# Kernel optimization log

Hardware: AMD Instinct MI355X
Metric: run time of the kernel (lower is better)

Reference implementation:

```python
import jax, jax.numpy as jnp
import numpy as np

KS = 3   # window kernel size
NH = 4   # num heads

def unfold3d(x, ks):
    # x: (B,C,D,H,W) -> (B,C,D*H*W, ks**3); matches torch unfold(2).unfold(3).unfold(4) ordering
    B, C, D, H, W = x.shape
    p = ks // 2
    xp = jnp.pad(x, ((0,0),(0,0),(p,p),(p,p),(p,p)))
    wins = [xp[:, :, i:i+D, j:j+H, k:k+W]
            for i in range(ks) for j in range(ks) for k in range(ks)]
    u = jnp.stack(wins, axis=-1)  # (B,C,D,H,W,ks^3)
    return u.reshape(B, C, D*H*W, ks**3)

def make_mask(D, H, W, ks):
    ones = jnp.ones((1, 1, D, H, W), jnp.float32)
    return unfold3d(ones, ks)[0, 0] == 0  # (N, ks^3), True = out-of-bounds (masked)

def l2norm(x, eps=1e-12):
    n = jnp.sqrt(jnp.sum(x * x, axis=-1, keepdims=True))
    return x / jnp.maximum(n, eps)

def layernorm(x, g, b, eps=1e-5):
    m = x.mean(-1, keepdims=True)
    v = x.var(-1, keepdims=True)
    return (x - m) / jnp.sqrt(v + eps) * g + b

def conv3d(x, w, b, pad):
    y = jax.lax.conv_general_dilated(x, w, (1,1,1), [(pad,pad)]*3,
        dimension_numbers=('NCDHW', 'OIDHW', 'NCDHW'))
    return y + b.reshape(1, -1, 1, 1, 1)

def bnorm(x, g, b, eps=1e-5):
    # BatchNorm3d, training-mode batch statistics (biased variance)
    m = x.mean(axis=(0,2,3,4), keepdims=True)
    v = ((x - m) ** 2).mean(axis=(0,2,3,4), keepdims=True)
    return (x - m) / jnp.sqrt(v + eps) * g.reshape(1,-1,1,1,1) + b.reshape(1,-1,1,1,1)

def lrelu(x):
    return jnp.where(x > 0, x, 0.01 * x)

def resblock(x, w1, b1, g1, be1, w2, b2, g2, be2):
    # monai UnetResBlock, in==out, stride 1 -> identity residual
    y = lrelu(bnorm(conv3d(x, w1, b1, 1), g1, be1))
    y = bnorm(conv3d(y, w2, b2, 1), g2, be2)
    return lrelu(y + x)

def epa(x, D, H, W, mask, qkvv_w, temp, temp2, rpb, qemb, op1_w, op1_b, op2_w, op2_b):
    B, N, C = x.shape
    hd = C // NH
    qkvv = (x @ qkvv_w.T).reshape(B, N, 4, NH, hd).transpose(2, 0, 3, 1, 4)  # (4,B,NH,N,hd)
    q, k, v_ca, v_sa = qkvv[0], qkvv[1], qkvv[2], qkvv[3]
    # ---- spatial (local window) attention ----
    qns = (l2norm(q) + qemb) * jax.nn.softplus(temp2)  # (B,NH,N,hd)
    k_flat = k.transpose(0, 1, 3, 2).reshape(B, C, N)
    v_flat = v_sa.transpose(0, 1, 3, 2).reshape(B, C, N)
    k_loc = unfold3d(k_flat.reshape(B, C, D, H, W), KS).reshape(B, NH, hd, N, KS**3).transpose(0, 1, 3, 2, 4)
    v_loc = unfold3d(v_flat.reshape(B, C, D, H, W), KS).reshape(B, NH, hd, N, KS**3).transpose(0, 1, 3, 2, 4)
    attn_sa = jnp.einsum('bhnd,bhndk->bhnk', qns, k_loc) + rpb[None, :, None, :]
    attn_sa = jnp.where(mask[None, None], -jnp.inf, attn_sa)
    attn_sa = jax.nn.softmax(attn_sa, axis=-1)
    # NOTE: original torch code reshapes (B,NH,N,hd) directly to (B,N,C); replicate exactly
    x_sa = jnp.einsum('bhnk,bhndk->bhnd', attn_sa, v_loc).reshape(B, N, C)
    # ---- channel (cosine) cross-attention ----
    qt = l2norm(q.transpose(0, 1, 3, 2))  # (B,NH,hd,N), normalized over N
    kt = l2norm(k.transpose(0, 1, 3, 2))
    attn_ca = jax.nn.softmax(jnp.einsum('bhdn,bhen->bhde', qt, kt) * temp, axis=-1)
    x_ca = jnp.einsum('bhde,bhen->bhdn', attn_ca, v_ca.transpose(0, 1, 3, 2)).transpose(0, 3, 1, 2).reshape(B, N, C)
    return jnp.concatenate([x_sa @ op1_w.T + op1_b, x_ca @ op2_w.T + op2_b], axis=-1)


def setup_inputs() -> dict:
    key = jax.random.key(0)
    B, C, H, W, D = 1, 64, 32, 32, 32
    hd = C // NH
    ks = iter(jax.random.split(key, 40))
    def nrm(shape, s=0.02):
        return jax.random.normal(next(ks), shape, jnp.float32) * s
    inp = {
        'x': jax.random.normal(next(ks), (B, C, H, W, D), jnp.float32),
        'ln_g': jnp.ones((C,), jnp.float32), 'ln_b': jnp.zeros((C,), jnp.float32),
        'gamma': 1e-6 * jnp.ones((C,), jnp.float32),
        'qkvv_w': nrm((4 * C, C)),
        'temp': jnp.ones((NH, 1, 1), jnp.float32), 'temp2': jnp.ones((NH, 1, 1), jnp.float32),
        'rpb': nrm((NH, KS**3), 4e-4),
        'qemb': nrm((NH, 1, hd)),
        'op1_w': nrm((C // 2, C)), 'op1_b': jnp.zeros((C // 2,), jnp.float32),
        'op2_w': nrm((C // 2, C)), 'op2_b': jnp.zeros((C // 2,), jnp.float32),
    }
    for name in ('c51', 'c52'):
        inp[name + '_w1'] = nrm((C, C, 3, 3, 3)); inp[name + '_b1'] = jnp.zeros((C,), jnp.float32)
        inp[name + '_g1'] = jnp.ones((C,), jnp.float32); inp[name + '_be1'] = jnp.zeros((C,), jnp.float32)
        inp[name + '_w2'] = nrm((C, C, 3, 3, 3)); inp[name + '_b2'] = jnp.zeros((C,), jnp.float32)
        inp[name + '_g2'] = jnp.ones((C,), jnp.float32); inp[name + '_be2'] = jnp.zeros((C,), jnp.float32)
    inp['c8_w'] = nrm((C, C, 1, 1, 1)); inp['c8_b'] = jnp.zeros((C,), jnp.float32)
    return inp


def reference(x, ln_g, ln_b, gamma, qkvv_w, temp, temp2, rpb, qemb,
              op1_w, op1_b, op2_w, op2_b,
              c51_w1, c51_b1, c51_g1, c51_be1, c51_w2, c51_b2, c51_g2, c51_be2,
              c52_w1, c52_b1, c52_g1, c52_be1, c52_w2, c52_b2, c52_g2, c52_be2,
              c8_w, c8_b):
    B, C, H, W, D = x.shape
    N = H * W * D
    xs = x.reshape(B, C, N).transpose(0, 2, 1)  # (B,N,C)
    mask = make_mask(D, H, W, KS)
    attn = xs + gamma * epa(layernorm(xs, ln_g, ln_b), D, H, W, mask,
                            qkvv_w, temp, temp2, rpb, qemb, op1_w, op1_b, op2_w, op2_b)
    skip = attn.reshape(B, H, W, D, C).transpose(0, 4, 1, 2, 3)  # (B,C,H,W,D)
    y = resblock(skip, c51_w1, c51_b1, c51_g1, c51_be1, c51_w2, c51_b2, c51_g2, c51_be2)
    y = resblock(y, c52_w1, c52_b1, c52_g1, c52_be1, c52_w2, c52_b2, c52_g2, c52_be2)
    return skip + conv3d(y, c8_w, c8_b, 0)
```

## Files before the change

kernel.cpp:

```cpp
#include <hip/hip_runtime.h>
#include <hip/hip_bf16.h>

typedef __hip_bfloat16 bf16;
typedef __attribute__((ext_vector_type(8))) short s8v;
typedef __attribute__((ext_vector_type(4))) float f4v;

#define NTOT 32768
#define HSZ ((size_t)NTOT*16)

__device__ __forceinline__ float bflo(unsigned int u){ union{unsigned int i;float f;}v; v.i=u<<16; return v.f; }
__device__ __forceinline__ float bfhi(unsigned int u){ union{unsigned int i;float f;}v; v.i=u&0xffff0000u; return v.f; }
__device__ __forceinline__ unsigned short f2bu(float f){ bf16 h = __float2bfloat16(f); unsigned short s; __builtin_memcpy(&s,&h,2); return s; }
__device__ __forceinline__ unsigned int pk2(float a, float b){ return (unsigned int)f2bu(a) | ((unsigned int)f2bu(b)<<16); }

__device__ __forceinline__ void load16(const bf16* p, float* o){
  const uint4* q = (const uint4*)p;
  uint4 u0 = q[0], u1 = q[1];
  o[0]=bflo(u0.x); o[1]=bfhi(u0.x); o[2]=bflo(u0.y); o[3]=bfhi(u0.y);
  o[4]=bflo(u0.z); o[5]=bfhi(u0.z); o[6]=bflo(u0.w); o[7]=bfhi(u0.w);
  o[8]=bflo(u1.x); o[9]=bfhi(u1.x); o[10]=bflo(u1.y); o[11]=bfhi(u1.y);
  o[12]=bflo(u1.z); o[13]=bfhi(u1.z); o[14]=bflo(u1.w); o[15]=bfhi(u1.w);
}

__global__ __launch_bounds__(256) void k_qkvv(const float* __restrict__ x,
    const float* __restrict__ lng, const float* __restrict__ lnb,
    const float* __restrict__ w,
    bf16* __restrict__ Qh, bf16* __restrict__ Kh, bf16* __restrict__ Vsh, bf16* __restrict__ Vch)
{
  __shared__ unsigned char sm[64000];
  float* xt = (float*)sm;
  float* mean_s = (float*)(sm + 16896);
  float* rstd_s = (float*)(sm + 16896 + 256);
  float* g_s    = (float*)(sm + 16896 + 512);
  float* b_s    = (float*)(sm + 16896 + 768);
  unsigned char* A2 = sm + 17920;
  unsigned char* Wb = sm + 27136;
  unsigned char* Cout = sm;

  int t = threadIdx.x;
  int n0 = blockIdx.x * 64;
  #pragma unroll
  for (int i=0;i<4;i++){
    int idx = t + i*256; int c = idx>>4, g = idx&15;
    *(float4*)&xt[c*66 + g*4] = *(const float4*)(x + (size_t)c*NTOT + n0 + g*4);
  }
  #pragma unroll
  for (int i=0;i<8;i++){
    int idx = t + i*256; int j = idx>>3, g = idx&7;
    float4 wa = *(const float4*)(w + (size_t)j*64 + g*8);
    float4 wb = *(const float4*)(w + (size_t)j*64 + g*8 + 4);
    uint4 u; u.x=pk2(wa.x,wa.y); u.y=pk2(wa.z,wa.w); u.z=pk2(wb.x,wb.y); u.w=pk2(wb.z,wb.w);
    *(uint4*)(Wb + j*144 + g*16) = u;
  }
  if (t<64){ g_s[t]=lng[t]; b_s[t]=lnb[t]; }
  __syncthreads();
  if (t<64){
    float s=0.f, ss=0.f;
    for (int c=0;c<64;c++){ float v=xt[c*66+t]; s+=v; ss+=v*v; }
    float m = s*(1.f/64.f);
    float var = ss*(1.f/64.f) - m*m;
    mean_s[t]=m; rstd_s[t]=rsqrtf(var+1e-5f);
  }
  __syncthreads();
  {
    int p = t>>2, c0 = (t&3)*16;
    float m = mean_s[p], rs = rstd_s[p];
    unsigned short tmp[16];
    #pragma unroll
    for (int i=0;i<16;i++){
      int c = c0+i;
      tmp[i] = f2bu((xt[c*66+p]-m)*rs*g_s[c] + b_s[c]);
    }
    *(uint4*)(A2 + p*144 + c0*2)      = *(uint4*)&tmp[0];
    *(uint4*)(A2 + p*144 + c0*2 + 16) = *(uint4*)&tmp[8];
  }
  __syncthreads();
  int wv = t>>6, lane = t&63, r = lane&15, q = lane>>4;
  f4v acc[4][4];
  #pragma unroll
  for (int mt=0;mt<4;mt++)
    #pragma unroll
    for (int nt=0;nt<4;nt++){ acc[mt][nt][0]=0.f; acc[mt][nt][1]=0.f; acc[mt][nt][2]=0.f; acc[mt][nt][3]=0.f; }
  #pragma unroll
  for (int ks=0; ks<2; ++ks){
    s8v af[4], bfr[4];
    #pragma unroll
    for (int mt=0;mt<4;mt++) af[mt] = *(const s8v*)(A2 + (mt*16+r)*144 + ks*64 + q*16);
    #pragma unroll
    for (int nt=0;nt<4;nt++) bfr[nt] = *(const s8v*)(Wb + ((wv*4+nt)*16+r)*144 + ks*64 + q*16);
    #pragma unroll
    for (int mt=0;mt<4;mt++)
      #pragma unroll
      for (int nt=0;nt<4;nt++)
        acc[mt][nt] = __builtin_amdgcn_mfma_f32_16x16x32_bf16(af[mt], bfr[nt], acc[mt][nt], 0, 0, 0);
  }
  __syncthreads();
  #pragma unroll
  for (int mt=0;mt<4;mt++)
    #pragma unroll
    for (int nt=0;nt<4;nt++){
      int j = (wv*4+nt)*16 + r;
      #pragma unroll
      for (int reg=0;reg<4;reg++){
        int p = mt*16 + q*4 + reg;
        *(unsigned short*)(Cout + p*528 + j*2) = f2bu(acc[mt][nt][reg]);
      }
    }
  __syncthreads();
  bf16* bases[4] = {Qh, Kh, Vch, Vsh};
  #pragma unroll
  for (int k=0;k<4;k++){
    int chunk = t + k*256;
    int combo = chunk >> 6, pos = chunk & 63;
    int tensor = combo >> 2, h = combo & 3;
    uint4 v = *(const uint4*)(Cout + pos*528 + (tensor*64 + h*16)*2);
    *(uint4*)((unsigned char*)bases[tensor] + ((size_t)h*HSZ + (size_t)(n0+pos)*16)*2) = v;
  }
}

__global__ __launch_bounds__(256) void k_chanpart(const bf16* __restrict__ Qh, const bf16* __restrict__ Kh,
    float* __restrict__ G, float* __restrict__ NQ, float* __restrict__ NK)
{
  int h = blockIdx.y;
  int t = threadIdx.x; int d = t>>4, e = t&15;
  __shared__ float qs[128][16];
  __shared__ float ks[128][16];
  float acc=0.f, accq=0.f, acck=0.f;
  for (int stage=0; stage<4; ++stage){
    int n0 = blockIdx.x*512 + stage*128;
    __syncthreads();
    {
      int row = t & 127, which = t >> 7;
      const bf16* p = (which ? Kh : Qh) + ((size_t)h*NTOT + n0 + row)*16;
      float tmp[16]; load16(p, tmp);
      float* dst = which ? &ks[row][0] : &qs[row][0];
      #pragma unroll
      for (int i=0;i<16;i++) dst[i]=tmp[i];
    }
    __syncthreads();
    for (int i=0;i<128;i++){
      float qv = qs[i][d], kv = ks[i][e];
      acc += qv*kv;
      if (e==0) accq += qv*qv;
      if (e==1){ float kd = ks[i][d]; acck += kd*kd; }
    }
  }
  atomicAdd(&G[(h*16+d)*16+e], acc);
  if (e==0) atomicAdd(&NQ[h*16+d], accq);
  if (e==1) atomicAdd(&NK[h*16+d], acck);
}

__global__ __launch_bounds__(256) void k_spatial(const bf16* __restrict__ Qh, const bf16* __restrict__ Kh,
    const bf16* __restrict__ Vsh, const bf16* __restrict__ Vch,
    const float* __restrict__ G, const float* __restrict__ NQ, const float* __restrict__ NK,
    const float* __restrict__ temp, const float* __restrict__ temp2,
    const float* __restrict__ rpb, const float* __restrict__ qemb,
    const float* __restrict__ x,
    const float* __restrict__ op1w, const float* __restrict__ op1b,
    const float* __restrict__ op2w, const float* __restrict__ op2b,
    const float* __restrict__ gamma, float* __restrict__ skipf)
{
  __shared__ float aca_s[1024];
  __shared__ float rpb_s[108];
  __shared__ float qemb_s[64];
  __shared__ float xs_s[64][68];
  __shared__ float xc_s[64][68];
  int t = threadIdx.x;
  int n0 = blockIdx.x * 64;
  if (t < 64){
    int hh = t>>4;
    float tp = temp[hh];
    float nq = fmaxf(sqrtf(NQ[t]), 1e-12f);
    float sv[16]; float mx=-3.0e38f;
    #pragma unroll
    for (int e=0;e<16;e++){
      float nk = fmaxf(sqrtf(NK[hh*16+e]), 1e-12f);
      sv[e] = G[t*16+e] / (nq*nk) * tp;
      mx = fmaxf(mx, sv[e]);
    }
    float sum=0.f;
    #pragma unroll
    for (int e=0;e<16;e++){ sv[e]=expf(sv[e]-mx); sum+=sv[e]; }
    float inv = 1.f/sum;
    #pragma unroll
    for (int e=0;e<16;e++) aca_s[t*16+e] = sv[e]*inv;
  }
  if (t<108) rpb_s[t]=rpb[t];
  if (t<64) qemb_s[t]=qemb[t];
  __syncthreads();
  int lane = t & 63, h = t >> 6;
  int n = n0 + lane;
  int a = n>>10, b=(n>>5)&31, c=n&31;
  const bf16* Kb = Kh + (size_t)h*HSZ;
  const bf16* Vb = Vsh + (size_t)h*HSZ;
  float q[16]; load16(Qh + (size_t)h*HSZ + (size_t)n*16, q);
  float s2=0.f;
  #pragma unroll
  for (int d=0;d<16;d++) s2 += q[d]*q[d];
  float inv = 1.f/fmaxf(sqrtf(s2), 1e-12f);
  float st2 = log1pf(expf(temp2[h]));
  #pragma unroll
  for (int d=0;d<16;d++) q[d] = (q[d]*inv + qemb_s[h*16+d])*st2;
  float sc[27]; float mx = -3.0e38f;
  #pragma unroll
  for (int kk=0;kk<27;kk++){
    int da=kk/9-1, db=(kk/3)%3-1, dc=kk%3-1;
    int aa=a+da, bb=b+db, cc=c+dc;
    float s = -3.0e38f;
    if ((unsigned)aa<32u && (unsigned)bb<32u && (unsigned)cc<32u){
      int nn = n + da*1024 + db*32 + dc;
      float kv[16]; load16(Kb + (size_t)nn*16, kv);
      s = rpb_s[h*27+kk];
      #pragma unroll
      for (int d=0;d<16;d++) s += q[d]*kv[d];
    }
    sc[kk]=s; mx = fmaxf(mx, s);
  }
  float sum=0.f;
  #pragma unroll
  for (int kk=0;kk<27;kk++){ float e = expf(sc[kk]-mx); sc[kk]=e; sum+=e; }
  float invs = 1.f/sum;
  float o[16];
  #pragma unroll
  for (int d=0;d<16;d++) o[d]=0.f;
  #pragma unroll
  for (int kk=0;kk<27;kk++){
    int da=kk/9-1, db=(kk/3)%3-1, dc=kk%3-1;
    int aa=a+da, bb=b+db, cc=c+dc;
    if ((unsigned)aa<32u && (unsigned)bb<32u && (unsigned)cc<32u){
      int nn = n + da*1024 + db*32 + dc;
      float vv[16]; load16(Vb + (size_t)nn*16, vv);
      float p = sc[kk];
      #pragma unroll
      for (int d=0;d<16;d++) o[d] += p*vv[d];
    }
  }
  {
    int jrow = h*16 + (lane>>2), cbase = (lane&3)*16;
    #pragma unroll
    for (int d=0;d<16;d++) xs_s[jrow][cbase + d] = o[d]*invs;
  }
  {
    float vca[16]; load16(Vch + (size_t)h*HSZ + (size_t)n*16, vca);
    #pragma unroll
    for (int d=0;d<16;d++){
      float s=0.f;
      #pragma unroll
      for (int e=0;e<16;e++) s += aca_s[(h*16+d)*16+e]*vca[e];
      xc_s[lane][h*16+d] = s;
    }
  }
  __syncthreads();
  int co = t & 63, pg = t >> 6;
  const float* wrow = (co < 32) ? (op1w + (size_t)co*64) : (op2w + (size_t)(co-32)*64);
  float wreg[64];
  #pragma unroll
  for (int i=0;i<16;i++) *(float4*)&wreg[i*4] = *(const float4*)(wrow + i*4);
  float bv = (co<32) ? op1b[co] : op2b[co-32];
  float gv = gamma[co];
  const float* xt_ = (co<32) ? &xs_s[0][0] : &xc_s[0][0];
  #pragma unroll
  for (int i=0;i<16;i++){
    int p = pg*16 + i;
    const float* xr = xt_ + p*68;
    float s = bv;
    #pragma unroll
    for (int k4=0;k4<16;k4++){
      float4 xv = *(const float4*)(xr + k4*4);
      s += wreg[k4*4]*xv.x + wreg[k4*4+1]*xv.y + wreg[k4*4+2]*xv.z + wreg[k4*4+3]*xv.w;
    }
    int m;
    if (co < 32){ int hh2 = p>>4, jj = p&15; m = hh2*8192 + (n0>>2) + jj; }
    else m = n0 + p;
    skipf[(size_t)m*64 + co] = x[(size_t)co*NTOT + m] + gv*s;
  }
}

__global__ void k_wprep(const float* __restrict__ wA, const float* __restrict__ wB_,
    const float* __restrict__ wC, const float* __restrict__ wD,
    const float* __restrict__ w8, bf16* __restrict__ WB, float* __restrict__ w8t,
    float* __restrict__ statz)
{
  int idx = blockIdx.x*256 + threadIdx.x;
  if (idx < 1152) statz[idx] = 0.f;
  if (idx < 458752){
    int j = idx & 7;
    int rr = (idx>>3) & 15;
    int q = (idx>>7) & 3;
    int nt = (idx>>9) & 3;
    int rest = idx >> 11;
    int tp = rest % 14;
    int rest2 = rest / 14;
    int cc = rest2 & 3;
    int conv = rest2 >> 2;
    int co = nt*16 + rr;
    int tap = 2*tp + (q>>1);
    int ci = cc*16 + (q&1)*8 + j;
    const float* src = conv==0?wA:conv==1?wB_:conv==2?wC:wD;
    float v = (tap < 27) ? src[((size_t)co*64 + ci)*27 + tap] : 0.f;
    WB[idx] = __float2bfloat16(v);
  }
  if (idx < 4096){ int ci = idx>>6, co = idx&63; w8t[ci*64+co] = w8[(size_t)co*64+ci]; }
}

template<int MODE>
__global__ __launch_bounds__(256, 2) void k_conv3x(const void* __restrict__ src,
    const float* __restrict__ stats, const float* __restrict__ g, const float* __restrict__ be,
    const float* __restrict__ resid,
    const bf16* __restrict__ WB, const float* __restrict__ bias,
    bf16* __restrict__ Yout, float* __restrict__ BNpart)
{
  __shared__ float smf[17408];
  unsigned char* smb = (unsigned char*)smf;
  int t = threadIdx.x;
  int w = t >> 6, lane = t & 63;
  int r = lane & 15, q = lane >> 4;
  int qe = q & 1, qh = q >> 1;
  int a = blockIdx.x >> 4, b0 = (blockIdx.x & 15) * 2;
  int hh = t & 7;

  float m8[8], rs8[8], be8[8];
  if (MODE != 0){
    #pragma unroll
    for (int i=0;i<8;i++){
      int ci = hh*8 + i;
      float S = stats[ci*2], SS = stats[ci*2+1];
      float m = S*(1.f/NTOT);
      m8[i] = m;
      rs8[i] = rsqrtf(SS*(1.f/NTOT) - m*m + 1e-5f) * g[ci];
      be8[i] = be[ci];
    }
  }

  if (MODE == 0){
    #pragma unroll
    for (int c0=0;c0<2;++c0){
      int kb = c0*7, kn = (c0==0)?7:6;
      float4 f0[7], f1[7]; int fl[7];
      #pragma unroll
      for (int k=0;k<7;k++){
        fl[k]=0;
        if (k<kn){
          int idx = t + (kb+k)*256;
          if (idx < 3264){
            int pos = idx>>3;
            int par=pos/136, rem=pos-par*136, pbr=rem/34, pc=rem-pbr*34;
            int pa=a+par, pb=b0+pbr;
            fl[k]=1;
            if (pa>=1&&pa<=32&&pb>=1&&pb<=32&&pc>=1&&pc<=32){
              int nsrc=(pa-1)*1024+(pb-1)*32+(pc-1);
              const float* p = (const float*)src + (size_t)nsrc*64 + hh*8;
              f0[k]=*(const float4*)p; f1[k]=*(const float4*)(p+4);
              fl[k]=2;
            }
          }
        }
      }
      #pragma unroll
      for (int k=0;k<7;k++){
        if (k<kn && fl[k]){
          int pos = (t + (kb+k)*256)>>3;
          uint4 o={0,0,0,0};
          if (fl[k]==2){
            o.x=pk2(f0[k].x,f0[k].y); o.y=pk2(f0[k].z,f0[k].w);
            o.z=pk2(f1[k].x,f1[k].y); o.w=pk2(f1[k].z,f1[k].w);
          }
          *(uint4*)(smb + pos*144 + hh*16) = o;
        }
      }
    }
  } else {
    const int CS = (MODE==2)?5:13;
    const int NC = (MODE==2)?3:1;
    #pragma unroll
    for (int c0=0;c0<NC;++c0){
      int kb = c0*CS;
      int kn = (MODE==2) ? ((c0==2)?3:5) : 13;
      uint4 u[CS]; float4 r0[CS], r1[CS]; int fl[CS];
      #pragma unroll
      for (int k=0;k<CS;k++){
        fl[k]=0;
        if (k<kn){
          int idx = t + (kb+k)*256;
          if (idx < 3264){
            int pos = idx>>3;
            int par=pos/136, rem=pos-par*136, pbr=rem/34, pc=rem-pbr*34;
            int pa=a+par, pb=b0+pbr;
            fl[k]=1;
            if (pa>=1&&pa<=32&&pb>=1&&pb<=32&&pc>=1&&pc<=32){
              int nsrc=(pa-1)*1024+(pb-1)*32+(pc-1);
              u[k] = *(const uint4*)((const unsigned char*)src + ((size_t)nsrc*64 + hh*8)*2);
              if (MODE==2){
                const float* rp = resid + (size_t)nsrc*64 + hh*8;
                r0[k]=*(const float4*)rp; r1[k]=*(const float4*)(rp+4);
              }
              fl[k]=2;
            }
          }
        }
      }
      #pragma unroll
      for (int k=0;k<CS;k++){
        if (k<kn && fl[k]){
          int pos = (t + (kb+k)*256)>>3;
          uint4 o={0,0,0,0};
          if (fl[k]==2){
            float v[8];
            v[0]=bflo(u[k].x); v[1]=bfhi(u[k].x); v[2]=bflo(u[k].y); v[3]=bfhi(u[k].y);
            v[4]=bflo(u[k].z); v[5]=bfhi(u[k].z); v[6]=bflo(u[k].w); v[7]=bfhi(u[k].w);
            float rv[8];
            if (MODE==2){
              rv[0]=r0[k].x; rv[1]=r0[k].y; rv[2]=r0[k].z; rv[3]=r0[k].w;
              rv[4]=r1[k].x; rv[5]=r1[k].y; rv[6]=r1[k].z; rv[7]=r1[k].w;
            }
            #pragma unroll
            for (int i=0;i<8;i++){
              float y = (v[i]-m8[i])*rs8[i] + be8[i];
              if (MODE==2) y += rv[i];
              v[i] = y>0.f ? y : 0.01f*y;
            }
            o.x=pk2(v[0],v[1]); o.y=pk2(v[2],v[3]); o.z=pk2(v[4],v[5]); o.w=pk2(v[6],v[7]);
          }
          *(uint4*)(smb + pos*144 + hh*16) = o;
        }
      }
    }
  }

  int toff[14];
  #pragma unroll
  for (int tp=0;tp<14;++tp){
    int tap = 2*tp + qh;
    int da = tap/9, rem = tap - da*9, db = rem/3, dc = rem - db*3;
    toff[tp] = (tap<27) ? (((da*4+db)*34 + dc)*144) : 0;
  }
  int F[4];
  #pragma unroll
  for (int mt=0;mt<4;mt++) F[mt] = (((mt>>1)*34 + (mt&1)*16 + r)*144) + w*32 + qe*16;
  const unsigned char* wbp = (const unsigned char*)WB + (size_t)w*57344 + lane*16;

  f4v acc[4][4];
  #pragma unroll
  for (int mt=0;mt<4;mt++)
    #pragma unroll
    for (int nt=0;nt<4;nt++){ acc[mt][nt][0]=0.f; acc[mt][nt][1]=0.f; acc[mt][nt][2]=0.f; acc[mt][nt][3]=0.f; }

  __syncthreads();

  s8v aC[4], bC[4], bN[4];
  #pragma unroll
  for (int mt=0;mt<4;mt++) aC[mt] = *(const s8v*)(smb + F[mt] + toff[0]);
  #pragma unroll
  for (int nt=0;nt<4;nt++){ bC[nt] = *(const s8v*)(wbp + nt*1024); bN[nt] = *(const s8v*)(wbp + 4096 + nt*1024); }

  #pragma unroll
  for (int tp=0; tp<14; ++tp){
    s8v aN[4], bN2[4];
    if (tp < 12){
      #pragma unroll
      for (int nt=0;nt<4;nt++) bN2[nt] = *(const s8v*)(wbp + (tp+2)*4096 + nt*1024);
    }
    if (tp < 13){
      #pragma unroll
      for (int mt=0;mt<4;mt++) aN[mt] = *(const s8v*)(smb + F[mt] + toff[tp+1]);
    }
    #pragma unroll
    for (int mt=0;mt<4;mt++)
      #pragma unroll
      for (int nt=0;nt<4;nt++)
        acc[mt][nt] = __builtin_amdgcn_mfma_f32_16x16x32_bf16(aC[mt], bC[nt], acc[mt][nt], 0, 0, 0);
    #pragma unroll
    for (int nt=0;nt<4;nt++) bC[nt] = bN[nt];
    if (tp < 12){
      #pragma unroll
      for (int nt=0;nt<4;nt++) bN[nt] = bN2[nt];
    }
    if (tp < 13){
      #pragma unroll
      for (int mt=0;mt<4;mt++) aC[mt] = aN[mt];
    }
  }

  __syncthreads();
  #pragma unroll
  for (int mt=0;mt<4;mt++)
    #pragma unroll
    for (int nt=0;nt<4;nt++)
      *(float4*)&smf[w*4352 + (nt*16+r)*68 + mt*16 + q*4] = *(float4*)&acc[mt][nt];
  __syncthreads();

  float vals[16];
  {
    int co = t >> 2, pg = t & 3;
    float bv = bias[co];
    #pragma unroll
    for (int i4=0;i4<4;i4++){
      int p = pg*16 + i4*4;
      float4 s0 = *(const float4*)&smf[0*4352 + co*68 + p];
      float4 s1 = *(const float4*)&smf[1*4352 + co*68 + p];
      float4 s2 = *(const float4*)&smf[2*4352 + co*68 + p];
      float4 s3 = *(const float4*)&smf[3*4352 + co*68 + p];
      vals[i4*4+0] = s0.x+s1.x+s2.x+s3.x+bv;
      vals[i4*4+1] = s0.y+s1.y+s2.y+s3.y+bv;
      vals[i4*4+2] = s0.z+s1.z+s2.z+s3.z+bv;
      vals[i4*4+3] = s0.w+s1.w+s2.w+s3.w+bv;
    }
    float s=0.f, ss=0.f;
    #pragma unroll
    for (int i=0;i<16;i++){ s+=vals[i]; ss+=vals[i]*vals[i]; }
    s += __shfl_xor(s,1); ss += __shfl_xor(ss,1);
    s += __shfl_xor(s,2); ss += __shfl_xor(ss,2);
    if (pg==0){
      BNpart[(size_t)blockIdx.x*128 + co*2]     = s;
      BNpart[(size_t)blockIdx.x*128 + co*2 + 1] = ss;
    }
  }
  __syncthreads();
  {
    int co = t >> 2, pg = t & 3;
    #pragma unroll
    for (int i=0;i<16;i++) smf[(pg*16+i)*68 + co] = vals[i];
  }
  __syncthreads();
  {
    int pos = t >> 2, grp = t & 3;
    float v16[16];
    #pragma unroll
    for (int i4=0;i4<4;i4++) *(float4*)&v16[i4*4] = *(const float4*)&smf[pos*68 + grp*16 + i4*4];
    uint4 u0, u1;
    u0.x=pk2(v16[0],v16[1]); u0.y=pk2(v16[2],v16[3]); u0.z=pk2(v16[4],v16[5]); u0.w=pk2(v16[6],v16[7]);
    u1.x=pk2(v16[8],v16[9]); u1.y=pk2(v16[10],v16[11]); u1.z=pk2(v16[12],v16[13]); u1.w=pk2(v16[14],v16[15]);
    int nb = a*1024 + (b0 + (pos>>5))*32 + (pos&31);
    uint4* dst = (uint4*)((unsigned char*)Yout + ((size_t)nb*64 + grp*16)*2);
    dst[0] = u0; dst[1] = u1;
  }
}

__global__ __launch_bounds__(1024) void k_bnred(const float* __restrict__ BNpart, float* __restrict__ BNout)
{
  __shared__ float red[8][128];
  int t = threadIdx.x;
  int col = t & 127, grp = t >> 7;
  float acc = 0.f;
  #pragma unroll 8
  for (int r = grp*64; r < grp*64 + 64; ++r) acc += BNpart[r*128 + col];
  red[grp][col] = acc;
  __syncthreads();
  if (grp == 0){
    float s = 0.f;
    #pragma unroll
    for (int g=0; g<8; g++) s += red[g][col];
    BNout[col] = s;
  }
}

__global__ __launch_bounds__(256) void k_conv1f(const bf16* __restrict__ Y4,
    const float* __restrict__ BN4, const float* __restrict__ g4, const float* __restrict__ be4,
    const bf16* __restrict__ Y2, const float* __restrict__ BN2,
    const float* __restrict__ g2, const float* __restrict__ be2,
    const float* __restrict__ skipf, const float* __restrict__ w8t, const float* __restrict__ b8,
    float* __restrict__ out)
{
  __shared__ float R2[64][68];
  __shared__ float skT[64][68];
  __shared__ float wt[4096];
  __shared__ float bs[64];
  int t = threadIdx.x;
  int n0 = blockIdx.x * 64;
  #pragma unroll
  for (int k=0;k<4;k++){
    int idx = t + k*256;
    *(float4*)&wt[idx*4] = *(const float4*)(w8t + idx*4);
  }
  if (t < 64) bs[t] = b8[t];
  {
    int pos = t >> 2, grp = t & 3;
    int n = n0 + pos;
    float y2[16], y4[16], sk[16];
    load16(Y2 + (size_t)n*64 + grp*16, y2);
    load16(Y4 + (size_t)n*64 + grp*16, y4);
    #pragma unroll
    for (int i4=0;i4<4;i4++) *(float4*)&sk[i4*4] = *(const float4*)(skipf + (size_t)n*64 + grp*16 + i4*4);
    #pragma unroll
    for (int i=0;i<16;i++){
      int ci = grp*16+i;
      float S2=BN2[ci*2], SS2=BN2[ci*2+1];
      float m2=S2*(1.f/NTOT);
      float r2v=rsqrtf(SS2*(1.f/NTOT)-m2*m2+1e-5f);
      float R = (y2[i]-m2)*r2v*g2[ci]+be2[ci] + sk[i];
      R = R>0.f ? R : 0.01f*R;
      float S4=BN4[ci*2], SS4=BN4[ci*2+1];
      float m4=S4*(1.f/NTOT);
      float r4v=rsqrtf(SS4*(1.f/NTOT)-m4*m4+1e-5f);
      float vy = (y4[i]-m4)*r4v*g4[ci]+be4[ci] + R;
      vy = vy>0.f ? vy : 0.01f*vy;
      R2[ci][pos] = vy;
      skT[ci][pos] = sk[i];
    }
  }
  __syncthreads();
  int lane = t & 63, cg = t >> 6;
  float acc[16];
  #pragma unroll
  for (int j=0;j<16;j++) acc[j]=0.f;
  for (int ci=0; ci<64; ci++){
    float rv = R2[ci][lane];
    const float* wr = &wt[ci*64 + cg*16];
    float4 wa = *(const float4*)(wr);
    float4 wb = *(const float4*)(wr+4);
    float4 wc = *(const float4*)(wr+8);
    float4 wd = *(const float4*)(wr+12);
    acc[0]+=rv*wa.x; acc[1]+=rv*wa.y; acc[2]+=rv*wa.z; acc[3]+=rv*wa.w;
    acc[4]+=rv*wb.x; acc[5]+=rv*wb.y; acc[6]+=rv*wb.z; acc[7]+=rv*wb.w;
    acc[8]+=rv*wc.x; acc[9]+=rv*wc.y; acc[10]+=rv*wc.z; acc[11]+=rv*wc.w;
    acc[12]+=rv*wd.x; acc[13]+=rv*wd.y; acc[14]+=rv*wd.z; acc[15]+=rv*wd.w;
  }
  #pragma unroll
  for (int j=0;j<16;j++){
    int co = cg*16+j;
    out[(size_t)co*NTOT + n0 + lane] = acc[j] + bs[co] + skT[co][lane];
  }
}

extern "C" void kernel_launch(void* const* d_in, const int* in_sizes, int n_in,
                              void* d_out, int out_size, void* d_ws, size_t ws_size,
                              hipStream_t stream) {
  (void)in_sizes; (void)n_in; (void)out_size; (void)ws_size;
  const float* x      = (const float*)d_in[0];
  const float* ln_g   = (const float*)d_in[1];
  const float* ln_b   = (const float*)d_in[2];
  const float* gamma  = (const float*)d_in[3];
  const float* qkvv_w = (const float*)d_in[4];
  const float* temp   = (const float*)d_in[5];
  const float* temp2  = (const float*)d_in[6];
  const float* rpb    = (const float*)d_in[7];
  const float* qemb   = (const float*)d_in[8];
  const float* op1w   = (const float*)d_in[9];
  const float* op1b   = (const float*)d_in[10];
  const float* op2w   = (const float*)d_in[11];
  const float* op2b   = (const float*)d_in[12];
  const float* c51_w1 = (const float*)d_in[13];
  const float* c51_b1 = (const float*)d_in[14];
  const float* c51_g1 = (const float*)d_in[15];
  const float* c51_be1= (const float*)d_in[16];
  const float* c51_w2 = (const float*)d_in[17];
  const float* c51_b2 = (const float*)d_in[18];
  const float* c51_g2 = (const float*)d_in[19];
  const float* c51_be2= (const float*)d_in[20];
  const float* c52_w1 = (const float*)d_in[21];
  const float* c52_b1 = (const float*)d_in[22];
  const float* c52_g1 = (const float*)d_in[23];
  const float* c52_be1= (const float*)d_in[24];
  const float* c52_w2 = (const float*)d_in[25];
  const float* c52_b2 = (const float*)d_in[26];
  const float* c52_g2 = (const float*)d_in[27];
  const float* c52_be2= (const float*)d_in[28];
  const float* c8_w   = (const float*)d_in[29];
  const float* c8_b   = (const float*)d_in[30];

  unsigned char* ws = (unsigned char*)d_ws;
  const size_t MB = 1u<<20;
  bf16*  Qh   = (bf16*)(ws + 0);
  bf16*  Kh   = (bf16*)(ws + 4*MB);
  bf16*  Vsh  = (bf16*)(ws + 8*MB);
  bf16*  Vch  = (bf16*)(ws + 12*MB);
  float* skipf= (float*)(ws + 24*MB);
  float* stat = (float*)(ws + 32*MB);
  float* G    = stat + 0;
  float* NQ   = stat + 1024;
  float* NK   = stat + 1088;
  float* BN1  = stat + 1152;
  float* BN2  = stat + 1312;
  float* BN3  = stat + 1472;
  float* BN4  = stat + 1632;
  bf16*  WB   = (bf16*)(ws + 33*MB);
  float* w8t  = (float*)(ws + 33*MB + 1048576);
  float* BNpart = (float*)(ws + 35*MB);
  bf16*  Y1   = (bf16*)(ws + 36*MB);
  bf16*  Y2   = (bf16*)(ws + 40*MB);
  bf16*  Y3   = (bf16*)(ws + 44*MB);
  bf16*  Y4   = (bf16*)(ws + 48*MB);

  k_wprep<<<1792,256,0,stream>>>(c51_w1, c51_w2, c52_w1, c52_w2, c8_w, WB, w8t, stat);
  k_qkvv<<<512,256,0,stream>>>(x, ln_g, ln_b, qkvv_w, Qh, Kh, Vsh, Vch);
  k_chanpart<<<dim3(64,4),256,0,stream>>>(Qh, Kh, G, NQ, NK);
  k_spatial<<<512,256,0,stream>>>(Qh, Kh, Vsh, Vch, G, NQ, NK, temp, temp2, rpb, qemb,
                                  x, op1w, op1b, op2w, op2b, gamma, skipf);
  k_conv3x<0><<<512,256,0,stream>>>(skipf, nullptr, nullptr, nullptr, nullptr, WB + 0*114688, c51_b1, Y1, BNpart);
  k_bnred<<<1,1024,0,stream>>>(BNpart, BN1);
  k_conv3x<1><<<512,256,0,stream>>>(Y1, BN1, c51_g1, c51_be1, nullptr, WB + 1*114688, c51_b2, Y2, BNpart);
  k_bnred<<<1,1024,0,stream>>>(BNpart, BN2);
  k_conv3x<2><<<512,256,0,stream>>>(Y2, BN2, c51_g2, c51_be2, skipf, WB + 2*114688, c52_b1, Y3, BNpart);
  k_bnred<<<1,1024,0,stream>>>(BNpart, BN3);
  k_conv3x<1><<<512,256,0,stream>>>(Y3, BN3, c52_g1, c52_be1, nullptr, WB + 3*114688, c52_b2, Y4, BNpart);
  k_bnred<<<1,1024,0,stream>>>(BNpart, BN4);
  k_conv1f<<<512,256,0,stream>>>(Y4, BN4, c52_g2, c52_be2, Y2, BN2, c51_g2, c51_be2, skipf, w8t, c8_b, (float*)d_out);
}
```

Baseline: 288.3 us.

## Split conv3x input channels into two halves to cut LDS and raise occupancy

The 3x3x3 conv kernel now stages the input tile in two 32-channel halves instead of all 64 channels at once, shrinking shared memory from about 68KB to 36KB and raising launch bounds to 4 blocks per CU. Work is redistributed so each wave owns one row pair and one channel sub-slice with 2x4 accumulators instead of 4x4, lowering register pressure. The cross-wave reduction sums two partials instead of four. In exchange it adds an extra staging phase with an extra barrier and drops the two-deep weight prefetch to one-deep.

Result: slower. 354.9 us (+23.1%).

```diff
diff --git a/kernel.cpp b/kernel.cpp
--- a/kernel.cpp
+++ b/kernel.cpp
@@ -304,206 +304,167 @@
 }
 
 template<int MODE>
-__global__ __launch_bounds__(256, 2) void k_conv3x(const void* __restrict__ src,
+__global__ __launch_bounds__(256, 4) void k_conv3x(const void* __restrict__ src,
     const float* __restrict__ stats, const float* __restrict__ g, const float* __restrict__ be,
     const float* __restrict__ resid,
     const bf16* __restrict__ WB, const float* __restrict__ bias,
     bf16* __restrict__ Yout, float* __restrict__ BNpart)
 {
-  __shared__ float smf[17408];
+  __shared__ float smf[9216];
   unsigned char* smb = (unsigned char*)smf;
   int t = threadIdx.x;
   int w = t >> 6, lane = t & 63;
   int r = lane & 15, q = lane >> 4;
   int qe = q & 1, qh = q >> 1;
+  int p = w >> 1, kw = w & 1;
   int a = blockIdx.x >> 4, b0 = (blockIdx.x & 15) * 2;
-  int hh = t & 7;
-
-  float m8[8], rs8[8], be8[8];
-  if (MODE != 0){
-    #pragma unroll
-    for (int i=0;i<8;i++){
-      int ci = hh*8 + i;
-      float S = stats[ci*2], SS = stats[ci*2+1];
-      float m = S*(1.f/NTOT);
-      m8[i] = m;
-      rs8[i] = rsqrtf(SS*(1.f/NTOT) - m*m + 1e-5f) * g[ci];
-      be8[i] = be[ci];
-    }
-  }
-
-  if (MODE == 0){
-    #pragma unroll
-    for (int c0=0;c0<2;++c0){
-      int kb = c0*7, kn = (c0==0)?7:6;
-      float4 f0[7], f1[7]; int fl[7];
-      #pragma unroll
-      for (int k=0;k<7;k++){
-        fl[k]=0;
-        if (k<kn){
-          int idx = t + (kb+k)*256;
-          if (idx < 3264){
-            int pos = idx>>3;
-            int par=pos/136, rem=pos-par*136, pbr=rem/34, pc=rem-pbr*34;
-            int pa=a+par, pb=b0+pbr;
-            fl[k]=1;
+
+  int toff[14];
+  #pragma unroll
+  for (int tp=0;tp<14;++tp){
+    int tap = 2*tp + qh;
+    int da = tap/9, rem = tap - da*9, db = rem/3, dc = rem - db*3;
+    toff[tp] = (tap<27) ? (((da*4+db)*34 + dc)*80) : 0;
+  }
+  int F0 = (p*34 + r)*80 + kw*32 + qe*16;
+  int F1 = F0 + 16*80;
+
+  f4v acc[2][4];
+  #pragma unroll
+  for (int mtl=0;mtl<2;mtl++)
+    #pragma unroll
+    for (int nt=0;nt<4;nt++){ acc[mtl][nt][0]=0.f; acc[mtl][nt][1]=0.f; acc[mtl][nt][2]=0.f; acc[mtl][nt][3]=0.f; }
+
+  #pragma unroll
+  for (int h=0; h<2; ++h){
+    float m8[8], rs8[8], be8[8];
+    if (MODE != 0){
+      int hq = t & 3;
+      #pragma unroll
+      for (int i=0;i<8;i++){
+        int ci = h*32 + hq*8 + i;
+        float S = stats[ci*2], SS = stats[ci*2+1];
+        float m = S*(1.f/NTOT);
+        m8[i] = m;
+        rs8[i] = rsqrtf(SS*(1.f/NTOT) - m*m + 1e-5f) * g[ci];
+        be8[i] = be[ci];
+      }
+    }
+    if (h == 1) __syncthreads();
+    #pragma unroll
+    for (int g2=0; g2<2; ++g2){
+      uint4 u[4]; float4 f0[4], f1[4]; int fl[4];
+      #pragma unroll
+      for (int k=0;k<4;k++){
+        int kk = g2*4 + k; fl[k]=0;
+        if (kk < 7){
+          int idx = t + kk*256;
+          if (idx < 1632){
+            int pos = idx >> 2, hq2 = idx & 3;
+            int par = pos/136, rem2 = pos - par*136, pbr = rem2/34, pc = rem2 - pbr*34;
+            int pa = a + par, pb = b0 + pbr;
+            fl[k] = 1;
             if (pa>=1&&pa<=32&&pb>=1&&pb<=32&&pc>=1&&pc<=32){
-              int nsrc=(pa-1)*1024+(pb-1)*32+(pc-1);
-              const float* p = (const float*)src + (size_t)nsrc*64 + hh*8;
-              f0[k]=*(const float4*)p; f1[k]=*(const float4*)(p+4);
-              fl[k]=2;
+              int nsrc = (pa-1)*1024 + (pb-1)*32 + (pc-1);
+              if (MODE == 0){
+                const float* pp = (const float*)src + (size_t)nsrc*64 + h*32 + hq2*8;
+                f0[k] = *(const float4*)pp; f1[k] = *(const float4*)(pp+4);
+              } else {
+                u[k] = *(const uint4*)((const unsigned char*)src + ((size_t)nsrc*64 + h*32 + hq2*8)*2);
+                if (MODE == 2){
+                  const float* rp = resid + (size_t)nsrc*64 + h*32 + hq2*8;
+                  f0[k] = *(const float4*)rp; f1[k] = *(const float4*)(rp+4);
+                }
+              }
+              fl[k] = 2;
             }
           }
         }
       }
       #pragma unroll
-      for (int k=0;k<7;k++){
-        if (k<kn && fl[k]){
-          int pos = (t + (kb+k)*256)>>3;
-          uint4 o={0,0,0,0};
-          if (fl[k]==2){
-            o.x=pk2(f0[k].x,f0[k].y); o.y=pk2(f0[k].z,f0[k].w);
-            o.z=pk2(f1[k].x,f1[k].y); o.w=pk2(f1[k].z,f1[k].w);
+      for (int k=0;k<4;k++){
+        int kk = g2*4 + k;
+        if (kk < 7 && fl[k]){
+          int idx = t + kk*256;
+          int pos = idx >> 2, hq2 = idx & 3;
+          uint4 o = {0,0,0,0};
+          if (fl[k] == 2){
+            if (MODE == 0){
+              o.x = pk2(f0[k].x, f0[k].y); o.y = pk2(f0[k].z, f0[k].w);
+              o.z = pk2(f1[k].x, f1[k].y); o.w = pk2(f1[k].z, f1[k].w);
+            } else {
+              float v[8];
+              v[0]=bflo(u[k].x); v[1]=bfhi(u[k].x); v[2]=bflo(u[k].y); v[3]=bfhi(u[k].y);
+              v[4]=bflo(u[k].z); v[5]=bfhi(u[k].z); v[6]=bflo(u[k].w); v[7]=bfhi(u[k].w);
+              float rv[8];
+              if (MODE==2){
+                rv[0]=f0[k].x; rv[1]=f0[k].y; rv[2]=f0[k].z; rv[3]=f0[k].w;
+                rv[4]=f1[k].x; rv[5]=f1[k].y; rv[6]=f1[k].z; rv[7]=f1[k].w;
+              }
+              #pragma unroll
+              for (int i=0;i<8;i++){
+                float y = (v[i]-m8[i])*rs8[i] + be8[i];
+                if (MODE==2) y += rv[i];
+                v[i] = y>0.f ? y : 0.01f*y;
+              }
+              o.x=pk2(v[0],v[1]); o.y=pk2(v[2],v[3]); o.z=pk2(v[4],v[5]); o.w=pk2(v[6],v[7]);
+            }
           }
-          *(uint4*)(smb + pos*144 + hh*16) = o;
+          *(uint4*)(smb + pos*80 + hq2*16) = o;
         }
       }
     }
-  } else {
-    const int CS = (MODE==2)?5:13;
-    const int NC = (MODE==2)?3:1;
-    #pragma unroll
-    for (int c0=0;c0<NC;++c0){
-      int kb = c0*CS;
-      int kn = (MODE==2) ? ((c0==2)?3:5) : 13;
-      uint4 u[CS]; float4 r0[CS], r1[CS]; int fl[CS];
-      #pragma unroll
-      for (int k=0;k<CS;k++){
-        fl[k]=0;
-        if (k<kn){
-          int idx = t + (kb+k)*256;
-          if (idx < 3264){
-            int pos = idx>>3;
-            int par=pos/136, rem=pos-par*136, pbr=rem/34, pc=rem-pbr*34;
-            int pa=a+par, pb=b0+pbr;
-            fl[k]=1;
-            if (pa>=1&&pa<=32&&pb>=1&&pb<=32&&pc>=1&&pc<=32){
-              int nsrc=(pa-1)*1024+(pb-1)*32+(pc-1);
-              u[k] = *(const uint4*)((const unsigned char*)src + ((size_t)nsrc*64 + hh*8)*2);
-              if (MODE==2){
-                const float* rp = resid + (size_t)nsrc*64 + hh*8;
-                r0[k]=*(const float4*)rp; r1[k]=*(const float4*)(rp+4);
-              }
-              fl[k]=2;
-            }
-          }
-        }
+    __syncthreads();
+    int cc = h*2 + kw;
+    const unsigned char* wbp = (const unsigned char*)WB + (size_t)cc*57344 + lane*16;
+    s8v aC0, aC1, bC[4];
+    aC0 = *(const s8v*)(smb + F0 + toff[0]);
+    aC1 = *(const s8v*)(smb + F1 + toff[0]);
+    #pragma unroll
+    for (int nt=0;nt<4;nt++) bC[nt] = *(const s8v*)(wbp + nt*1024);
+    #pragma unroll
+    for (int tp=0; tp<14; ++tp){
+      s8v aN0, aN1, bN[4];
+      if (tp < 13){
+        #pragma unroll
+        for (int nt=0;nt<4;nt++) bN[nt] = *(const s8v*)(wbp + (tp+1)*4096 + nt*1024);
+        aN0 = *(const s8v*)(smb + F0 + toff[tp+1]);
+        aN1 = *(const s8v*)(smb + F1 + toff[tp+1]);
       }
       #pragma unroll
-      for (int k=0;k<CS;k++){
-        if (k<kn && fl[k]){
-          int pos = (t + (kb+k)*256)>>3;
-          uint4 o={0,0,0,0};
-          if (fl[k]==2){
-            float v[8];
-            v[0]=bflo(u[k].x); v[1]=bfhi(u[k].x); v[2]=bflo(u[k].y); v[3]=bfhi(u[k].y);
-            v[4]=bflo(u[k].z); v[5]=bfhi(u[k].z); v[6]=bflo(u[k].w); v[7]=bfhi(u[k].w);
-            float rv[8];
-            if (MODE==2){
-              rv[0]=r0[k].x; rv[1]=r0[k].y; rv[2]=r0[k].z; rv[3]=r0[k].w;
-              rv[4]=r1[k].x; rv[5]=r1[k].y; rv[6]=r1[k].z; rv[7]=r1[k].w;
-            }
-            #pragma unroll
-            for (int i=0;i<8;i++){
-              float y = (v[i]-m8[i])*rs8[i] + be8[i];
-              if (MODE==2) y += rv[i];
-              v[i] = y>0.f ? y : 0.01f*y;
-            }
-            o.x=pk2(v[0],v[1]); o.y=pk2(v[2],v[3]); o.z=pk2(v[4],v[5]); o.w=pk2(v[6],v[7]);
-          }
-          *(uint4*)(smb + pos*144 + hh*16) = o;
-        }
+      for (int nt=0;nt<4;nt++){
+        acc[0][nt] = __builtin_amdgcn_mfma_f32_16x16x32_bf16(aC0, bC[nt], acc[0][nt], 0, 0, 0);
+        acc[1][nt] = __builtin_amdgcn_mfma_f32_16x16x32_bf16(aC1, bC[nt], acc[1][nt], 0, 0, 0);
       }
-    }
-  }
-
-  int toff[14];
-  #pragma unroll
-  for (int tp=0;tp<14;++tp){
-    int tap = 2*tp + qh;
-    int da = tap/9, rem = tap - da*9, db = rem/3, dc = rem - db*3;
-    toff[tp] = (tap<27) ? (((da*4+db)*34 + dc)*144) : 0;
-  }
-  int F[4];
-  #pragma unroll
-  for (int mt=0;mt<4;mt++) F[mt] = (((mt>>1)*34 + (mt&1)*16 + r)*144) + w*32 + qe*16;
-  const unsigned char* wbp = (const unsigned char*)WB + (size_t)w*57344 + lane*16;
-
-  f4v acc[4][4];
-  #pragma unroll
-  for (int mt=0;mt<4;mt++)
-    #pragma unroll
-    for (int nt=0;nt<4;nt++){ acc[mt][nt][0]=0.f; acc[mt][nt][1]=0.f; acc[mt][nt][2]=0.f; acc[mt][nt][3]=0.f; }
-
-  __syncthreads();
-
-  s8v aC[4], bC[4], bN[4];
-  #pragma unroll
-  for (int mt=0;mt<4;mt++) aC[mt] = *(const s8v*)(smb + F[mt] + toff[0]);
-  #pragma unroll
-  for (int nt=0;nt<4;nt++){ bC[nt] = *(const s8v*)(wbp + nt*1024); bN[nt] = *(const s8v*)(wbp + 4096 + nt*1024); }
-
-  #pragma unroll
-  for (int tp=0; tp<14; ++tp){
-    s8v aN[4], bN2[4];
-    if (tp < 12){
-      #pragma unroll
-      for (int nt=0;nt<4;nt++) bN2[nt] = *(const s8v*)(wbp + (tp+2)*4096 + nt*1024);
-    }
-    if (tp < 13){
-      #pragma unroll
-      for (int mt=0;mt<4;mt++) aN[mt] = *(const s8v*)(smb + F[mt] + toff[tp+1]);
-    }
-    #pragma unroll
-    for (int mt=0;mt<4;mt++)
-      #pragma unroll
-      for (int nt=0;nt<4;nt++)
-        acc[mt][nt] = __builtin_amdgcn_mfma_f32_16x16x32_bf16(aC[mt], bC[nt], acc[mt][nt], 0, 0, 0);
-    #pragma unroll
-    for (int nt=0;nt<4;nt++) bC[nt] = bN[nt];
-    if (tp < 12){
-      #pragma unroll
-      for (int nt=0;nt<4;nt++) bN[nt] = bN2[nt];
-    }
-    if (tp < 13){
-      #pragma unroll
-      for (int mt=0;mt<4;mt++) aC[mt] = aN[mt];
-    }
-  }
-
-  __syncthreads();
-  #pragma unroll
-  for (int mt=0;mt<4;mt++)
+      if (tp < 13){
+        #pragma unroll
+        for (int nt=0;nt<4;nt++) bC[nt] = bN[nt];
+        aC0 = aN0; aC1 = aN1;
+      }
+    }
+  }
+
+  __syncthreads();
+  #pragma unroll
+  for (int mtl=0;mtl<2;mtl++)
     #pragma unroll
     for (int nt=0;nt<4;nt++)
-      *(float4*)&smf[w*4352 + (nt*16+r)*68 + mt*16 + q*4] = *(float4*)&acc[mt][nt];
-  __syncthreads();
-
+      *(float4*)&smf[w*2304 + (nt*16+r)*36 + mtl*16 + q*4] = *(float4*)&acc[mtl][nt];
+  __syncthreads();
   float vals[16];
   {
     int co = t >> 2, pg = t & 3;
     float bv = bias[co];
     #pragma unroll
     for (int i4=0;i4<4;i4++){
-      int p = pg*16 + i4*4;
-      float4 s0 = *(const float4*)&smf[0*4352 + co*68 + p];
-      float4 s1 = *(const float4*)&smf[1*4352 + co*68 + p];
-      float4 s2 = *(const float4*)&smf[2*4352 + co*68 + p];
-      float4 s3 = *(const float4*)&smf[3*4352 + co*68 + p];
-      vals[i4*4+0] = s0.x+s1.x+s2.x+s3.x+bv;
-      vals[i4*4+1] = s0.y+s1.y+s2.y+s3.y+bv;
-      vals[i4*4+2] = s0.z+s1.z+s2.z+s3.z+bv;
-      vals[i4*4+3] = s0.w+s1.w+s2.w+s3.w+bv;
+      int pos = pg*16 + i4*4;
+      int ph = pos >> 5, c5 = pos & 31;
+      float4 s0 = *(const float4*)&smf[(ph*2+0)*2304 + co*36 + c5];
+      float4 s1 = *(const float4*)&smf[(ph*2+1)*2304 + co*36 + c5];
+      vals[i4*4+0] = s0.x+s1.x+bv;
+      vals[i4*4+1] = s0.y+s1.y+bv;
+      vals[i4*4+2] = s0.z+s1.z+bv;
+      vals[i4*4+3] = s0.w+s1.w+bv;
     }
     float s=0.f, ss=0.f;
     #pragma unroll
```
